# Kernel tuning notes

Hardware: AMD Instinct MI355X
Metric: run time of the kernel (lower is better)

The kernel has to match this reference:

```python
import jax, jax.numpy as jnp
import numpy as np

K = 3          # deformable kernel size
N = K * K      # sampling points per output pixel
PAD = 1
BN_EPS = 1e-5


def setup_inputs() -> dict:
    key = jax.random.key(0)
    ks = jax.random.split(key, 6)
    B, C, H, W = 32, 103, 32, 32
    Cout = 32
    x = jax.random.normal(ks[0], (B, C, H, W), jnp.float32)
    # offset-predicting conv: 2*N output channels (N y-offsets then N x-offsets)
    w_off = jax.random.normal(ks[1], (2 * N, C, K, K), jnp.float32) * 0.01
    b_off = jnp.zeros((2 * N,), jnp.float32)
    # main deformable conv weight
    w = jax.random.normal(ks[2], (Cout, C, K, K), jnp.float32) * (1.0 / np.sqrt(C * N))
    b = jnp.zeros((Cout,), jnp.float32)
    # BatchNorm (eval mode) params
    gamma = jax.random.uniform(ks[3], (Cout,), jnp.float32, 0.5, 1.5)
    beta = jax.random.normal(ks[4], (Cout,), jnp.float32) * 0.1
    run_mean = jax.random.normal(ks[5], (Cout,), jnp.float32) * 0.1
    run_var = jnp.ones((Cout,), jnp.float32)
    return {"x": x, "w_off": w_off, "b_off": b_off, "w": w, "b": b,
            "gamma": gamma, "beta": beta, "run_mean": run_mean, "run_var": run_var}


def _deform_conv(x, w_off, b_off, w, b):
    B, C, H, W = x.shape
    # predicted offsets: (B, 2N, H, W) -> (B, H, W, N) each for y and x
    off = jax.lax.conv_general_dilated(x, w_off, (1, 1), [(PAD, PAD), (PAD, PAD)])
    off = off + b_off[None, :, None, None]
    off_y = jnp.transpose(off[:, :N], (0, 2, 3, 1))
    off_x = jnp.transpose(off[:, N:], (0, 2, 3, 1))
    # regular kernel grid offsets p_n in {-1,0,1}^2
    ky, kx = jnp.meshgrid(jnp.arange(-1, 2, dtype=jnp.float32),
                          jnp.arange(-1, 2, dtype=jnp.float32), indexing='ij')
    kn_y, kn_x = ky.reshape(-1), kx.reshape(-1)  # (N,)
    # base grid p_0 in padded coordinates (stride 1, padding 1 -> starts at 1)
    p0_y = jnp.arange(1, H + 1, dtype=jnp.float32)[None, :, None, None]
    p0_x = jnp.arange(1, W + 1, dtype=jnp.float32)[None, None, :, None]
    Hp, Wp = H + 2 * PAD, W + 2 * PAD
    py = jnp.clip(p0_y + kn_y + off_y, 0.0, Hp - 1.0)  # (B,H,W,N)
    px = jnp.clip(p0_x + kn_x + off_x, 0.0, Wp - 1.0)
    # zero-padded input, flattened spatial for gather
    xp = jnp.pad(x, ((0, 0), (0, 0), (PAD, PAD), (PAD, PAD)))
    xf = xp.reshape(B, C, Hp * Wp)
    y0 = jnp.clip(jnp.floor(py).astype(jnp.int32), 0, Hp - 2)
    x0 = jnp.clip(jnp.floor(px).astype(jnp.int32), 0, Wp - 2)
    y1, x1 = y0 + 1, x0 + 1
    wy = (py - y0.astype(py.dtype))[:, None]  # (B,1,H,W,N)
    wx = (px - x0.astype(px.dtype))[:, None]

    def gather(yi, xi):
        idx = (yi * Wp + xi).reshape(B, -1)                      # (B, H*W*N)
        g = jnp.take_along_axis(xf, idx[:, None, :], axis=2)    # (B, C, H*W*N)
        return g.reshape(B, C, H, W, N)

    v00, v01 = gather(y0, x0), gather(y0, x1)
    v10, v11 = gather(y1, x0), gather(y1, x1)
    samp = (v00 * (1 - wy) * (1 - wx) + v01 * (1 - wy) * wx
            + v10 * wy * (1 - wx) + v11 * wy * wx)               # (B,C,H,W,N)
    out = jnp.einsum('bchwn,ocn->bohw', samp, w.reshape(w.shape[0], C, N))
    return out + b[None, :, None, None]


def reference(x, w_off, b_off, w, b, gamma, beta, run_mean, run_var):
    out = _deform_conv(x, w_off, b_off, w, b)
    # BatchNorm2d (eval mode) + ReLU
    inv = gamma * jax.lax.rsqrt(run_var + BN_EPS)
    out = out * inv[None, :, None, None] + (beta - run_mean * inv)[None, :, None, None]
    return jax.nn.relu(out)
```

## Files before the change

### kernel.cpp

```cpp
#include <hip/hip_runtime.h>


#define CC    103
#define COUT  32
#define NCHUNK 7
#define KSC   5
#define RSU   40
#define COLOFS 3
#define PLSU  1364
#define NPAIR 8
#define PLANES_U (NPAIR * PLSU)
#define WFRAG_U  2560

typedef __attribute__((ext_vector_type(8))) short bf16x8;
typedef __attribute__((ext_vector_type(4))) float f32x4;

#define WTPM_W 0
#define WTPO_W 17920
#define BN_W   35840

__device__ __forceinline__ unsigned short f2bf_rne(float f) {
    unsigned u = __float_as_uint(f);
    unsigned r = u + 0x7fffu + ((u >> 16) & 1u);
    return (unsigned short)(r >> 16);
}
__device__ __forceinline__ unsigned pack2(float s0, float s1) {
    unsigned u0 = __float_as_uint(s0) + 0x8000u;
    unsigned u1 = __float_as_uint(s1) + 0x8000u;
    return (u1 & 0xffff0000u) | (u0 >> 16);
}
__device__ __forceinline__ float blo(unsigned u) { return __uint_as_float(u << 16); }
__device__ __forceinline__ float bhi(unsigned u) { return __uint_as_float(u & 0xffff0000u); }

__global__ void k_prep(const float* __restrict__ w, const float* __restrict__ w_off,
                       const float* __restrict__ bias, const float* __restrict__ gamma,
                       const float* __restrict__ beta, const float* __restrict__ mean,
                       const float* __restrict__ var,
                       unsigned short* __restrict__ wtpm, unsigned short* __restrict__ wtpo,
                       float* __restrict__ bn) {
    int tid = blockIdx.x * 256 + threadIdx.x;
    if (tid < 71680) {
        int half = tid >= 35840 ? 1 : 0;
        int e = tid - half * 35840;
        const float* src = half ? w_off : w;
        unsigned short* dst = half ? wtpo : wtpm;
        int mrows = half ? 18 : 32;
        int j = e & 7, lane = (e >> 3) & 63, tile = e >> 9;
        int mt = tile & 1, chs = tile >> 1;
        int s = chs % 5, ch = chs / 5;
        int o = mt * 16 + (lane & 15);
        int kl = s * 32 + (lane >> 4) * 8 + j;
        int n = kl >> 4, c = ch * 16 + (kl & 15);
        float v = 0.f;
        if (n < 9 && c < CC && o < mrows) v = src[o * (CC * 9) + c * 9 + n];
        dst[e] = f2bf_rne(v);
    }
    if (tid < 32) {
        float inv = gamma[tid] * rsqrtf(var[tid] + 1e-5f);
        bn[tid]      = inv;
        bn[32 + tid] = beta[tid] + (bias[tid] - mean[tid]) * inv;
    }
}

__global__ void __launch_bounds__(256, 2)
k_fused(const float* __restrict__ x, const float* __restrict__ b_off,
        const unsigned short* __restrict__ wtpo, const unsigned short* __restrict__ wtpm,
        const float* __restrict__ bn, float* __restrict__ out) {
    __shared__ unsigned int ldsu[PLANES_U + WFRAG_U];
    __shared__ float exch[18 * 64];
    unsigned int* ldsw = ldsu + PLANES_U;

    int bid = blockIdx.x;
    int b   = (bid & 7) * 4 + ((bid >> 3) & 3);
    int pxg = bid >> 5;

    int t = threadIdx.x, lane = t & 63, wv = t >> 6;
    int pxl = wv * 16 + (lane & 15);
    int px  = pxg * 64 + pxl;
    int h = px >> 5, wq = px & 31;
    int hi = (lane >> 5) & 1;
    int quad = lane >> 4;
    int pb = (quad & 1) * 4;

    const int TAPL[5] = {0, 2, 4, 6, 8};
    const int TAPH[5] = {1, 3, 5, 7, 8};

    for (int i = t; i < PLANES_U; i += 256) ldsu[i] = 0u;

    const float* xb = x + b * (CC * 1024);
    int sr = t >> 3;
    int sc = (t & 7) * 4;

    f32x4 acc0 = {0.f, 0.f, 0.f, 0.f};
    f32x4 acc1 = {0.f, 0.f, 0.f, 0.f};
    for (int ch = 0; ch < NCHUNK; ch++) {
        __syncthreads();
        {
            const uint4* wsrc4 = (const uint4*)(wtpo + ch * 5120);
            for (int i = t; i < 640; i += 256) ((uint4*)ldsw)[i] = wsrc4[i];
        }
        {
            const float* srcb = xb + sr * 32 + sc;
            unsigned int* dstb = ldsu + (sr + 1) * RSU + COLOFS + 1 + sc;
#pragma unroll
            for (int i = 0; i < NPAIR; i++) {
                int c = ch * 16 + 2 * i;
                if (c < CC) {
                    float4 a = *(const float4*)(srcb + c * 1024);
                    float4 bb = make_float4(0.f, 0.f, 0.f, 0.f);
                    if (c + 1 < CC) bb = *(const float4*)(srcb + (c + 1) * 1024);
                    uint4 o4;
                    o4.x = pack2(a.x, bb.x); o4.y = pack2(a.y, bb.y);
                    o4.z = pack2(a.z, bb.z); o4.w = pack2(a.w, bb.w);
                    *(uint4*)(dstb + i * PLSU) = o4;
                }
            }
        }
        __syncthreads();
#pragma unroll
        for (int s = 0; s < KSC; s++) {
            int tap = hi ? TAPH[s] : TAPL[s];
            int ky = tap / 3, kx = tap % 3;
            const unsigned int* cell = ldsu + pb * PLSU + (h + ky) * RSU + COLOFS + (wq + kx);
            union { unsigned int u[4]; bf16x8 v; } bu;
#pragma unroll
            for (int jj = 0; jj < 4; jj++) bu.u[jj] = cell[jj * PLSU];
            bf16x8 a0 = *(const bf16x8*)(ldsw + s * 512 + lane * 4);
            bf16x8 a1 = *(const bf16x8*)(ldsw + s * 512 + 256 + lane * 4);
            acc0 = __builtin_amdgcn_mfma_f32_16x16x32_bf16(a0, bu.v, acc0, 0, 0, 0);
            acc1 = __builtin_amdgcn_mfma_f32_16x16x32_bf16(a1, bu.v, acc1, 0, 0, 0);
        }
    }

    __syncthreads();
    {
        float* ex = exch + pxl;
#pragma unroll
        for (int reg = 0; reg < 4; reg++) ex[(quad * 4 + reg) * 64] = acc0[reg];
        if (quad == 0) { ex[16 * 64] = acc1[0]; ex[17 * 64] = acc1[1]; }
    }
    {
        const uint4* wsrc4 = (const uint4*)(wtpm + 6 * 5120);
        for (int i = t; i < 640; i += 256) ((uint4*)ldsw)[i] = wsrc4[i];
    }
    __syncthreads();

    int   cofs[KSC];
    float wg[KSC][4];
#pragma unroll
    for (int s = 0; s < KSC; s++) {
        int tap = hi ? TAPH[s] : TAPL[s];
        float oy = exch[tap * 64 + pxl] + b_off[tap];
        float ox = exch[(9 + tap) * 64 + pxl] + b_off[9 + tap];
        float py  = (float)(h + tap / 3) + oy;
        float pxx = (float)(wq + tap % 3) + ox;
        py  = fminf(fmaxf(py, 0.f), 33.f);
        pxx = fminf(fmaxf(pxx, 0.f), 33.f);
        int y0 = min((int)py, 32);
        int x0 = min((int)pxx, 32);
        float fy = py - (float)y0;
        float fx = pxx - (float)x0;
        wg[s][0] = (1.f - fy) * (1.f - fx);
        wg[s][1] = (1.f - fy) * fx;
        wg[s][2] = fy * (1.f - fx);
        wg[s][3] = fy * fx;
        cofs[s] = pb * PLSU + y0 * RSU + COLOFS + x0;
    }

    acc0 = (f32x4){0.f, 0.f, 0.f, 0.f};
    acc1 = (f32x4){0.f, 0.f, 0.f, 0.f};
    for (int ch = NCHUNK - 1; ch >= 0; ch--) {
        if (ch != NCHUNK - 1) {
            __syncthreads();
            {
                const uint4* wsrc4 = (const uint4*)(wtpm + ch * 5120);
                for (int i = t; i < 640; i += 256) ((uint4*)ldsw)[i] = wsrc4[i];
            }
            {
                const float* srcb = xb + sr * 32 + sc;
                unsigned int* dstb = ldsu + (sr + 1) * RSU + COLOFS + 1 + sc;
#pragma unroll
                for (int i = 0; i < NPAIR; i++) {
                    int c = ch * 16 + 2 * i;
                    if (c < CC) {
                        float4 a = *(const float4*)(srcb + c * 1024);
                        float4 bb = make_float4(0.f, 0.f, 0.f, 0.f);
                        if (c + 1 < CC) bb = *(const float4*)(srcb + (c + 1) * 1024);
                        uint4 o4;
                        o4.x = pack2(a.x, bb.x); o4.y = pack2(a.y, bb.y);
                        o4.z = pack2(a.z, bb.z); o4.w = pack2(a.w, bb.w);
                        *(uint4*)(dstb + i * PLSU) = o4;
                    }
                }
            }
            __syncthreads();
        }
#pragma unroll
        for (int s = 0; s < KSC; s++) {
            const unsigned int* cell = ldsu + cofs[s];
            float w00 = wg[s][0], w01 = wg[s][1], w10 = wg[s][2], w11 = wg[s][3];
            union { unsigned int u[4]; bf16x8 v; } bu;
#pragma unroll
            for (int jj = 0; jj < 4; jj++) {
                unsigned t0 = cell[jj * PLSU];
                unsigned t1 = cell[jj * PLSU + 1];
                unsigned b0 = cell[jj * PLSU + RSU];
                unsigned b1 = cell[jj * PLSU + RSU + 1];
                float se = blo(t0) * w00;
                se = fmaf(blo(t1), w01, se);
                se = fmaf(blo(b0), w10, se);
                se = fmaf(blo(b1), w11, se);
                float so = bhi(t0) * w00;
                so = fmaf(bhi(t1), w01, so);
                so = fmaf(bhi(b0), w10, so);
                so = fmaf(bhi(b1), w11, so);
                bu.u[jj] = pack2(se, so);
            }
            bf16x8 a0 = *(const bf16x8*)(ldsw + s * 512 + lane * 4);
            bf16x8 a1 = *(const bf16x8*)(ldsw + s * 512 + 256 + lane * 4);
            acc0 = __builtin_amdgcn_mfma_f32_16x16x32_bf16(a0, bu.v, acc0, 0, 0, 0);
            acc1 = __builtin_amdgcn_mfma_f32_16x16x32_bf16(a1, bu.v, acc1, 0, 0, 0);
        }
    }

    const float* SC = bn;
    const float* SH = bn + 32;
    float* op = out + (size_t)b * COUT * 1024 + px;
#pragma unroll
    for (int mt = 0; mt < 2; mt++) {
        f32x4 a = mt ? acc1 : acc0;
#pragma unroll
        for (int reg = 0; reg < 4; reg++) {
            int o = mt * 16 + quad * 4 + reg;
            float v = a[reg] * SC[o] + SH[o];
            op[o * 1024] = fmaxf(v, 0.f);
        }
    }
}

extern "C" void kernel_launch(void* const* d_in, const int* in_sizes, int n_in,
                              void* d_out, int out_size, void* d_ws, size_t ws_size,
                              hipStream_t stream) {
    const float* x      = (const float*)d_in[0];
    const float* w_off  = (const float*)d_in[1];
    const float* b_off  = (const float*)d_in[2];
    const float* w      = (const float*)d_in[3];
    const float* bias   = (const float*)d_in[4];
    const float* gamma  = (const float*)d_in[5];
    const float* beta   = (const float*)d_in[6];
    const float* rmean  = (const float*)d_in[7];
    const float* rvar   = (const float*)d_in[8];
    float* out = (float*)d_out;

    float* ws = (float*)d_ws;
    unsigned short* wtpm = (unsigned short*)(ws + WTPM_W);
    unsigned short* wtpo = (unsigned short*)(ws + WTPO_W);
    float*          bn   = ws + BN_W;

    k_prep <<<280, 256, 0, stream>>>(w, w_off, bias, gamma, beta, rmean, rvar,
                                     wtpm, wtpo, bn);
    k_fused<<<512, 256, 0, stream>>>(x, b_off, wtpo, wtpm, bn, out);
}
```

Baseline: 123.6 us.

## Split channel chunks across two wave groups with fp16 packed bilinear sampling

Blocks grow to 512 threads, split into two groups of four waves. Each group takes alternate 16-channel chunks in its own LDS buffer, and the partial sums are reduced through shared memory for both the offset conv and the main conv. Bilinear interpolation now uses packed fp16 math with fp16 MFMA instead of scalar fp32 FMAs on bf16-unpacked values. Weight fragments are read straight from global memory instead of being staged in LDS. The change aims to double the latency hiding per block and cut ALU work per sample, at the cost of fp16 range/precision risk, extra reduction syncs, and global weight loads inside the MFMA loop.

```diff
diff --git a/kernel.cpp b/kernel.cpp
--- a/kernel.cpp
+++ b/kernel.cpp
@@ -3,34 +3,20 @@
 
 #define CC    103
 #define COUT  32
-#define NCHUNK 7
 #define KSC   5
-#define RSU   40
-#define COLOFS 3
-#define PLSU  1364
+#define RSU   34
+#define PLSU  1158
 #define NPAIR 8
-#define PLANES_U (NPAIR * PLSU)
-#define WFRAG_U  2560
-
-typedef __attribute__((ext_vector_type(8))) short bf16x8;
+#define BUF_U (NPAIR * PLSU)
+
+typedef __attribute__((ext_vector_type(8))) _Float16 f16x8;
+typedef __attribute__((ext_vector_type(2))) _Float16 h2;
+typedef __attribute__((ext_vector_type(2))) __fp16  fp16x2;
 typedef __attribute__((ext_vector_type(4))) float f32x4;
 
 #define WTPM_W 0
 #define WTPO_W 17920
 #define BN_W   35840
-
-__device__ __forceinline__ unsigned short f2bf_rne(float f) {
-    unsigned u = __float_as_uint(f);
-    unsigned r = u + 0x7fffu + ((u >> 16) & 1u);
-    return (unsigned short)(r >> 16);
-}
-__device__ __forceinline__ unsigned pack2(float s0, float s1) {
-    unsigned u0 = __float_as_uint(s0) + 0x8000u;
-    unsigned u1 = __float_as_uint(s1) + 0x8000u;
-    return (u1 & 0xffff0000u) | (u0 >> 16);
-}
-__device__ __forceinline__ float blo(unsigned u) { return __uint_as_float(u << 16); }
-__device__ __forceinline__ float bhi(unsigned u) { return __uint_as_float(u & 0xffff0000u); }
 
 __global__ void k_prep(const float* __restrict__ w, const float* __restrict__ w_off,
                        const float* __restrict__ bias, const float* __restrict__ gamma,
@@ -40,11 +26,11 @@
                        float* __restrict__ bn) {
     int tid = blockIdx.x * 256 + threadIdx.x;
     if (tid < 71680) {
-        int half = tid >= 35840 ? 1 : 0;
-        int e = tid - half * 35840;
-        const float* src = half ? w_off : w;
-        unsigned short* dst = half ? wtpo : wtpm;
-        int mrows = half ? 18 : 32;
+        int half_ = tid >= 35840 ? 1 : 0;
+        int e = tid - half_ * 35840;
+        const float* src = half_ ? w_off : w;
+        unsigned short* dst = half_ ? wtpo : wtpm;
+        int mrows = half_ ? 18 : 32;
         int j = e & 7, lane = (e >> 3) & 63, tile = e >> 9;
         int mt = tile & 1, chs = tile >> 1;
         int s = chs % 5, ch = chs / 5;
@@ -53,7 +39,9 @@
         int n = kl >> 4, c = ch * 16 + (kl & 15);
         float v = 0.f;
         if (n < 9 && c < CC && o < mrows) v = src[o * (CC * 9) + c * 9 + n];
-        dst[e] = f2bf_rne(v);
+        union { _Float16 h; unsigned short u; } cv;
+        cv.h = (_Float16)v;
+        dst[e] = cv.u;
     }
     if (tid < 32) {
         float inv = gamma[tid] * rsqrtf(var[tid] + 1e-5f);
@@ -62,178 +50,192 @@
     }
 }
 
-__global__ void __launch_bounds__(256, 2)
+__global__ void __launch_bounds__(512, 4)
 k_fused(const float* __restrict__ x, const float* __restrict__ b_off,
         const unsigned short* __restrict__ wtpo, const unsigned short* __restrict__ wtpm,
         const float* __restrict__ bn, float* __restrict__ out) {
-    __shared__ unsigned int ldsu[PLANES_U + WFRAG_U];
+    __shared__ unsigned int ldsp[2 * BUF_U];
     __shared__ float exch[18 * 64];
-    unsigned int* ldsw = ldsu + PLANES_U;
 
     int bid = blockIdx.x;
     int b   = (bid & 7) * 4 + ((bid >> 3) & 3);
     int pxg = bid >> 5;
 
     int t = threadIdx.x, lane = t & 63, wv = t >> 6;
-    int pxl = wv * 16 + (lane & 15);
+    int kh = wv >> 2;
+    int pw = wv & 3;
+    int pxl = pw * 16 + (lane & 15);
     int px  = pxg * 64 + pxl;
     int h = px >> 5, wq = px & 31;
-    int hi = (lane >> 5) & 1;
-    int quad = lane >> 4;
-    int pb = (quad & 1) * 4;
-
-    const int TAPL[5] = {0, 2, 4, 6, 8};
-    const int TAPH[5] = {1, 3, 5, 7, 8};
-
-    for (int i = t; i < PLANES_U; i += 256) ldsu[i] = 0u;
+    int kg = lane >> 4;
+    int hi = kg >> 1;
+    int pb = (kg & 1) * 4;
+
+    unsigned int* mybuf = ldsp + kh * BUF_U;
+
+    for (int i = t; i < 2 * BUF_U; i += 512) ldsp[i] = 0u;
 
     const float* xb = x + b * (CC * 1024);
-    int sr = t >> 3;
-    int sc = (t & 7) * 4;
+    int tl = t & 255;
+    int sr = tl >> 3, sk = (tl & 7) * 4;
+
+    const int KYL[5] = {0,0,1,2,2}, KXL[5] = {0,2,1,0,2};
+    const int KYH[5] = {0,1,1,2,2}, KXH[5] = {1,0,2,1,2};
+    const int TAPL[5] = {0,2,4,6,8}, TAPH[5] = {1,3,5,7,8};
+    int myky[5], mykx[5], mytap[5];
+#pragma unroll
+    for (int s = 0; s < 5; s++) {
+        myky[s] = hi ? KYH[s] : KYL[s];
+        mykx[s] = hi ? KXH[s] : KXL[s];
+        mytap[s] = hi ? TAPH[s] : TAPL[s];
+    }
+
+    auto stage = [&](int ch) {
+        const float* srcb = xb + sr * 32 + sk;
+        unsigned int* dstb = mybuf + (sr + 1) * RSU + 2 + sk;
+#pragma unroll
+        for (int i = 0; i < NPAIR; i++) {
+            int c = ch * 16 + 2 * i;
+            if (c < CC) {
+                float4 a = *(const float4*)(srcb + c * 1024);
+                float4 bb = make_float4(0.f, 0.f, 0.f, 0.f);
+                if (c + 1 < CC) bb = *(const float4*)(srcb + (c + 1) * 1024);
+                union { fp16x2 h; unsigned u; } p0, p1, p2, p3;
+                p0.h = __builtin_amdgcn_cvt_pkrtz(a.x, bb.x);
+                p1.h = __builtin_amdgcn_cvt_pkrtz(a.y, bb.y);
+                p2.h = __builtin_amdgcn_cvt_pkrtz(a.z, bb.z);
+                p3.h = __builtin_amdgcn_cvt_pkrtz(a.w, bb.w);
+                *(uint2*)(dstb + i * PLSU)     = make_uint2(p0.u, p1.u);
+                *(uint2*)(dstb + i * PLSU + 2) = make_uint2(p2.u, p3.u);
+            }
+        }
+    };
 
     f32x4 acc0 = {0.f, 0.f, 0.f, 0.f};
     f32x4 acc1 = {0.f, 0.f, 0.f, 0.f};
-    for (int ch = 0; ch < NCHUNK; ch++) {
+
+#pragma unroll
+    for (int it = 0; it < 4; it++) {
+        const int ch = kh ? (2 * it) : (it < 3 ? 2 * it + 1 : -1);
         __syncthreads();
-        {
-            const uint4* wsrc4 = (const uint4*)(wtpo + ch * 5120);
-            for (int i = t; i < 640; i += 256) ((uint4*)ldsw)[i] = wsrc4[i];
-        }
-        {
-            const float* srcb = xb + sr * 32 + sc;
-            unsigned int* dstb = ldsu + (sr + 1) * RSU + COLOFS + 1 + sc;
-#pragma unroll
-            for (int i = 0; i < NPAIR; i++) {
-                int c = ch * 16 + 2 * i;
-                if (c < CC) {
-                    float4 a = *(const float4*)(srcb + c * 1024);
-                    float4 bb = make_float4(0.f, 0.f, 0.f, 0.f);
-                    if (c + 1 < CC) bb = *(const float4*)(srcb + (c + 1) * 1024);
-                    uint4 o4;
-                    o4.x = pack2(a.x, bb.x); o4.y = pack2(a.y, bb.y);
-                    o4.z = pack2(a.z, bb.z); o4.w = pack2(a.w, bb.w);
-                    *(uint4*)(dstb + i * PLSU) = o4;
-                }
-            }
-        }
+        if (ch >= 0) stage(ch);
         __syncthreads();
-#pragma unroll
-        for (int s = 0; s < KSC; s++) {
-            int tap = hi ? TAPH[s] : TAPL[s];
-            int ky = tap / 3, kx = tap % 3;
-            const unsigned int* cell = ldsu + pb * PLSU + (h + ky) * RSU + COLOFS + (wq + kx);
-            union { unsigned int u[4]; bf16x8 v; } bu;
-#pragma unroll
-            for (int jj = 0; jj < 4; jj++) bu.u[jj] = cell[jj * PLSU];
-            bf16x8 a0 = *(const bf16x8*)(ldsw + s * 512 + lane * 4);
-            bf16x8 a1 = *(const bf16x8*)(ldsw + s * 512 + 256 + lane * 4);
-            acc0 = __builtin_amdgcn_mfma_f32_16x16x32_bf16(a0, bu.v, acc0, 0, 0, 0);
-            acc1 = __builtin_amdgcn_mfma_f32_16x16x32_bf16(a1, bu.v, acc1, 0, 0, 0);
-        }
-    }
-
-    __syncthreads();
-    {
+        if (ch >= 0) {
+            const unsigned short* wch = wtpo + ch * 5120;
+#pragma unroll
+            for (int s = 0; s < KSC; s++) {
+                const unsigned int* cell = mybuf + pb * PLSU
+                                         + (h + myky[s]) * RSU + 1 + (wq + mykx[s]);
+                union { unsigned u[4]; f16x8 v; } bu;
+#pragma unroll
+                for (int jj = 0; jj < 4; jj++) bu.u[jj] = cell[jj * PLSU];
+                f16x8 a0 = *(const f16x8*)(wch + s * 1024 + lane * 8);
+                f16x8 a1 = *(const f16x8*)(wch + s * 1024 + 512 + lane * 8);
+                acc0 = __builtin_amdgcn_mfma_f32_16x16x32_f16(a0, bu.v, acc0, 0, 0, 0);
+                acc1 = __builtin_amdgcn_mfma_f32_16x16x32_f16(a1, bu.v, acc1, 0, 0, 0);
+            }
+        }
+    }
+
+    __syncthreads();
+    if (kh == 0) {
         float* ex = exch + pxl;
 #pragma unroll
-        for (int reg = 0; reg < 4; reg++) ex[(quad * 4 + reg) * 64] = acc0[reg];
-        if (quad == 0) { ex[16 * 64] = acc1[0]; ex[17 * 64] = acc1[1]; }
-    }
-    {
-        const uint4* wsrc4 = (const uint4*)(wtpm + 6 * 5120);
-        for (int i = t; i < 640; i += 256) ((uint4*)ldsw)[i] = wsrc4[i];
-    }
-    __syncthreads();
-
-    int   cofs[KSC];
-    float wg[KSC][4];
+        for (int reg = 0; reg < 4; reg++) ex[(kg * 4 + reg) * 64] = acc0[reg];
+        if (kg == 0) { ex[16 * 64] = acc1[0]; ex[17 * 64] = acc1[1]; }
+    }
+    __syncthreads();
+    if (kh == 1) {
+        float* ex = exch + pxl;
+#pragma unroll
+        for (int reg = 0; reg < 4; reg++) ex[(kg * 4 + reg) * 64] += acc0[reg];
+        if (kg == 0) { ex[16 * 64] += acc1[0]; ex[17 * 64] += acc1[1]; }
+    }
+    __syncthreads();
+
+    int cofs[KSC];
+    h2  W[KSC][4];
 #pragma unroll
     for (int s = 0; s < KSC; s++) {
-        int tap = hi ? TAPH[s] : TAPL[s];
+        int tap = mytap[s];
         float oy = exch[tap * 64 + pxl] + b_off[tap];
         float ox = exch[(9 + tap) * 64 + pxl] + b_off[9 + tap];
-        float py  = (float)(h + tap / 3) + oy;
-        float pxx = (float)(wq + tap % 3) + ox;
+        float py  = (float)(h + myky[s]) + oy;
+        float pxx = (float)(wq + mykx[s]) + ox;
         py  = fminf(fmaxf(py, 0.f), 33.f);
         pxx = fminf(fmaxf(pxx, 0.f), 33.f);
         int y0 = min((int)py, 32);
         int x0 = min((int)pxx, 32);
         float fy = py - (float)y0;
         float fx = pxx - (float)x0;
-        wg[s][0] = (1.f - fy) * (1.f - fx);
-        wg[s][1] = (1.f - fy) * fx;
-        wg[s][2] = fy * (1.f - fx);
-        wg[s][3] = fy * fx;
-        cofs[s] = pb * PLSU + y0 * RSU + COLOFS + x0;
+        float w00 = (1.f - fy) * (1.f - fx), w01 = (1.f - fy) * fx;
+        float w10 = fy * (1.f - fx),          w11 = fy * fx;
+        W[s][0] = (h2){(_Float16)w00, (_Float16)w00};
+        W[s][1] = (h2){(_Float16)w01, (_Float16)w01};
+        W[s][2] = (h2){(_Float16)w10, (_Float16)w10};
+        W[s][3] = (h2){(_Float16)w11, (_Float16)w11};
+        cofs[s] = pb * PLSU + y0 * RSU + 1 + x0;
     }
 
     acc0 = (f32x4){0.f, 0.f, 0.f, 0.f};
     acc1 = (f32x4){0.f, 0.f, 0.f, 0.f};
-    for (int ch = NCHUNK - 1; ch >= 0; ch--) {
-        if (ch != NCHUNK - 1) {
+#pragma unroll
+    for (int it = 0; it < 4; it++) {
+        const int ch = kh ? (6 - 2 * it) : (it < 3 ? 5 - 2 * it : -1);
+        if (it > 0) {
             __syncthreads();
-            {
-                const uint4* wsrc4 = (const uint4*)(wtpm + ch * 5120);
-                for (int i = t; i < 640; i += 256) ((uint4*)ldsw)[i] = wsrc4[i];
-            }
-            {
-                const float* srcb = xb + sr * 32 + sc;
-                unsigned int* dstb = ldsu + (sr + 1) * RSU + COLOFS + 1 + sc;
-#pragma unroll
-                for (int i = 0; i < NPAIR; i++) {
-                    int c = ch * 16 + 2 * i;
-                    if (c < CC) {
-                        float4 a = *(const float4*)(srcb + c * 1024);
-                        float4 bb = make_float4(0.f, 0.f, 0.f, 0.f);
-                        if (c + 1 < CC) bb = *(const float4*)(srcb + (c + 1) * 1024);
-                        uint4 o4;
-                        o4.x = pack2(a.x, bb.x); o4.y = pack2(a.y, bb.y);
-                        o4.z = pack2(a.z, bb.z); o4.w = pack2(a.w, bb.w);
-                        *(uint4*)(dstb + i * PLSU) = o4;
-                    }
+            if (ch >= 0) stage(ch);
+            else {
+                float* ex2 = (float*)ldsp;
+                float* e = ex2 + pxl;
+#pragma unroll
+                for (int reg = 0; reg < 4; reg++) {
+                    e[(kg * 4 + reg) * 64]        = acc0[reg];
+                    e[(16 + kg * 4 + reg) * 64]   = acc1[reg];
                 }
             }
             __syncthreads();
         }
-#pragma unroll
-        for (int s = 0; s < KSC; s++) {
-            const unsigned int* cell = ldsu + cofs[s];
-            float w00 = wg[s][0], w01 = wg[s][1], w10 = wg[s][2], w11 = wg[s][3];
-            union { unsigned int u[4]; bf16x8 v; } bu;
-#pragma unroll
-            for (int jj = 0; jj < 4; jj++) {
-                unsigned t0 = cell[jj * PLSU];
-                unsigned t1 = cell[jj * PLSU + 1];
-                unsigned b0 = cell[jj * PLSU + RSU];
-                unsigned b1 = cell[jj * PLSU + RSU + 1];
-                float se = blo(t0) * w00;
-                se = fmaf(blo(t1), w01, se);
-                se = fmaf(blo(b0), w10, se);
-                se = fmaf(blo(b1), w11, se);
-                float so = bhi(t0) * w00;
-                so = fmaf(bhi(t1), w01, so);
-                so = fmaf(bhi(b0), w10, so);
-                so = fmaf(bhi(b1), w11, so);
-                bu.u[jj] = pack2(se, so);
-            }
-            bf16x8 a0 = *(const bf16x8*)(ldsw + s * 512 + lane * 4);
-            bf16x8 a1 = *(const bf16x8*)(ldsw + s * 512 + 256 + lane * 4);
-            acc0 = __builtin_amdgcn_mfma_f32_16x16x32_bf16(a0, bu.v, acc0, 0, 0, 0);
-            acc1 = __builtin_amdgcn_mfma_f32_16x16x32_bf16(a1, bu.v, acc1, 0, 0, 0);
-        }
-    }
-
-    const float* SC = bn;
-    const float* SH = bn + 32;
-    float* op = out + (size_t)b * COUT * 1024 + px;
-#pragma unroll
-    for (int mt = 0; mt < 2; mt++) {
-        f32x4 a = mt ? acc1 : acc0;
-#pragma unroll
-        for (int reg = 0; reg < 4; reg++) {
-            int o = mt * 16 + quad * 4 + reg;
-            float v = a[reg] * SC[o] + SH[o];
-            op[o * 1024] = fmaxf(v, 0.f);
+        if (ch >= 0) {
+            const unsigned short* wch = wtpm + ch * 5120;
+#pragma unroll
+            for (int s = 0; s < KSC; s++) {
+                const unsigned int* cell = mybuf + cofs[s];
+                union { unsigned u[4]; f16x8 v; } bu;
+#pragma unroll
+                for (int jj = 0; jj < 4; jj++) {
+                    union { unsigned u; h2 hh; } t0, t1, b0, b1;
+                    t0.u = cell[jj * PLSU];
+                    t1.u = cell[jj * PLSU + 1];
+                    b0.u = cell[jj * PLSU + RSU];
+                    b1.u = cell[jj * PLSU + RSU + 1];
+                    h2 sm = t0.hh * W[s][0] + t1.hh * W[s][1]
+                          + b0.hh * W[s][2] + b1.hh * W[s][3];
+                    union { h2 hh; unsigned u; } r; r.hh = sm;
+                    bu.u[jj] = r.u;
+                }
+                f16x8 a0 = *(const f16x8*)(wch + s * 1024 + lane * 8);
+                f16x8 a1 = *(const f16x8*)(wch + s * 1024 + 512 + lane * 8);
+                acc0 = __builtin_amdgcn_mfma_f32_16x16x32_f16(a0, bu.v, acc0, 0, 0, 0);
+                acc1 = __builtin_amdgcn_mfma_f32_16x16x32_f16(a1, bu.v, acc1, 0, 0, 0);
+            }
+        }
+    }
+
+    __syncthreads();
+    if (kh == 1) {
+        const float* ex2 = (const float*)ldsp;
+        float* op = out + (size_t)b * COUT * 1024 + px;
+#pragma unroll
+        for (int mt = 0; mt < 2; mt++) {
+            f32x4 a = mt ? acc1 : acc0;
+#pragma unroll
+            for (int reg = 0; reg < 4; reg++) {
+                int o = mt * 16 + kg * 4 + reg;
+                float tot = a[reg] + ex2[o * 64 + pxl];
+                float v = tot * bn[o] + bn[32 + o];
+                op[o * 1024] = fmaxf(v, 0.f);
+            }
         }
     }
 }
@@ -259,5 +261,5 @@
 
     k_prep <<<280, 256, 0, stream>>>(w, w_off, bias, gamma, beta, rmean, rvar,
                                      wtpm, wtpo, bn);
-    k_fused<<<512, 256, 0, stream>>>(x, b_off, wtpo, wtpm, bn, out);
+    k_fused<<<512, 512, 0, stream>>>(x, b_off, wtpo, wtpm, bn, out);
 }
```

Result: faster. 108.8 us (-12.0%).
